# Optimization experiments

Measured on AMD Instinct MI355X. Metric: run time of the kernel, lower is better.

Reference implementation:

```python
import jax, jax.numpy as jnp
import numpy as np

B, S_SRC, S_TGT = 32, 64, 1024
D, H, DFF, LE, LD, V = 128, 8, 512, 6, 6, 64


def _pe(S, d):
    # PyTorch-style sinusoidal positional encoding, shape [S, d]
    pos = np.arange(S, dtype=np.float32)[:, None]
    div = np.exp(np.arange(0, d, 2, dtype=np.float32) * (-np.log(10000.0) / d))
    pe = np.zeros((S, d), dtype=np.float32)
    pe[:, 0::2] = np.sin(pos * div)
    pe[:, 1::2] = np.cos(pos * div)
    return jnp.asarray(pe)


def _ln(x, g, b, eps=1e-5):
    m = x.mean(-1, keepdims=True)
    v = ((x - m) ** 2).mean(-1, keepdims=True)
    return (x - m) / jnp.sqrt(v + eps) * g + b


def _mha(q_in, k_in, v_in, Wqkv, bqkv, Wo, bo):
    d = q_in.shape[-1]
    dh = d // H
    def proj(x, W, b):
        return (x @ W.T + b).reshape(x.shape[0], x.shape[1], H, dh)
    q = proj(q_in, Wqkv[:d], bqkv[:d])
    k = proj(k_in, Wqkv[d:2 * d], bqkv[d:2 * d])
    v = proj(v_in, Wqkv[2 * d:], bqkv[2 * d:])
    scores = jnp.einsum('bqhd,bkhd->bhqk', q, k) * (1.0 / np.sqrt(dh))
    a = jax.nn.softmax(scores, axis=-1)
    o = jnp.einsum('bhqk,bkhd->bqhd', a, v).reshape(q_in.shape[0], q_in.shape[1], d)
    return o @ Wo.T + bo


def _ffn(x, W1, b1, W2, b2):
    return jax.nn.relu(x @ W1.T + b1) @ W2.T + b2


def reference(src, tgt, emb,
              enc_qkv_w, enc_qkv_b, enc_out_w, enc_out_b,
              enc_ln1_g, enc_ln1_b, enc_ff1_w, enc_ff1_b,
              enc_ff2_w, enc_ff2_b, enc_ln2_g, enc_ln2_b,
              enc_norm_g, enc_norm_b,
              dec_sa_qkv_w, dec_sa_qkv_b, dec_sa_out_w, dec_sa_out_b,
              dec_ln1_g, dec_ln1_b,
              dec_ca_qkv_w, dec_ca_qkv_b, dec_ca_out_w, dec_ca_out_b,
              dec_ln2_g, dec_ln2_b,
              dec_ff1_w, dec_ff1_b, dec_ff2_w, dec_ff2_b,
              dec_ln3_g, dec_ln3_b, dec_norm_g, dec_norm_b,
              fc_w, fc_b):
    # src: [B, S_SRC] int tokens (occupation config); tgt: [B, S_TGT, D] (zeros in the original)
    s = emb[src] * np.sqrt(float(D)) + _pe(src.shape[1], D)
    t = tgt + _pe(tgt.shape[1], D)
    # encoder (post-norm, ReLU, dropout=0 in eval)
    for i in range(LE):
        s = _ln(s + _mha(s, s, s, enc_qkv_w[i], enc_qkv_b[i], enc_out_w[i], enc_out_b[i]),
                enc_ln1_g[i], enc_ln1_b[i])
        s = _ln(s + _ffn(s, enc_ff1_w[i], enc_ff1_b[i], enc_ff2_w[i], enc_ff2_b[i]),
                enc_ln2_g[i], enc_ln2_b[i])
    mem = _ln(s, enc_norm_g, enc_norm_b)
    # decoder
    for i in range(LD):
        t = _ln(t + _mha(t, t, t, dec_sa_qkv_w[i], dec_sa_qkv_b[i], dec_sa_out_w[i], dec_sa_out_b[i]),
                dec_ln1_g[i], dec_ln1_b[i])
        t = _ln(t + _mha(t, mem, mem, dec_ca_qkv_w[i], dec_ca_qkv_b[i], dec_ca_out_w[i], dec_ca_out_b[i]),
                dec_ln2_g[i], dec_ln2_b[i])
        t = _ln(t + _ffn(t, dec_ff1_w[i], dec_ff1_b[i], dec_ff2_w[i], dec_ff2_b[i]),
                dec_ln3_g[i], dec_ln3_b[i])
    t = _ln(t, dec_norm_g, dec_norm_b)
    return t @ fc_w.T + fc_b  # [B, S_TGT, 1] transformer correction to TN params


def setup_inputs():
    ks = iter(jax.random.split(jax.random.key(0), 64))
    def nrm(shape, scale=0.02):
        return jax.random.normal(next(ks), shape, dtype=jnp.float32) * scale
    inp = {
        'src': jax.random.randint(next(ks), (B, S_SRC), 0, V),
        'tgt': jnp.zeros((B, S_TGT, D), jnp.float32),
        'emb': nrm((V, D), 1.0),
        'enc_qkv_w': nrm((LE, 3 * D, D)), 'enc_qkv_b': jnp.zeros((LE, 3 * D)),
        'enc_out_w': nrm((LE, D, D)), 'enc_out_b': jnp.zeros((LE, D)),
        'enc_ln1_g': jnp.ones((LE, D)), 'enc_ln1_b': jnp.zeros((LE, D)),
        'enc_ff1_w': nrm((LE, DFF, D)), 'enc_ff1_b': jnp.zeros((LE, DFF)),
        'enc_ff2_w': nrm((LE, D, DFF)), 'enc_ff2_b': jnp.zeros((LE, D)),
        'enc_ln2_g': jnp.ones((LE, D)), 'enc_ln2_b': jnp.zeros((LE, D)),
        'enc_norm_g': jnp.ones((D,)), 'enc_norm_b': jnp.zeros((D,)),
        'dec_sa_qkv_w': nrm((LD, 3 * D, D)), 'dec_sa_qkv_b': jnp.zeros((LD, 3 * D)),
        'dec_sa_out_w': nrm((LD, D, D)), 'dec_sa_out_b': jnp.zeros((LD, D)),
        'dec_ln1_g': jnp.ones((LD, D)), 'dec_ln1_b': jnp.zeros((LD, D)),
        'dec_ca_qkv_w': nrm((LD, 3 * D, D)), 'dec_ca_qkv_b': jnp.zeros((LD, 3 * D)),
        'dec_ca_out_w': nrm((LD, D, D)), 'dec_ca_out_b': jnp.zeros((LD, D)),
        'dec_ln2_g': jnp.ones((LD, D)), 'dec_ln2_b': jnp.zeros((LD, D)),
        'dec_ff1_w': nrm((LD, DFF, D)), 'dec_ff1_b': jnp.zeros((LD, DFF)),
        'dec_ff2_w': nrm((LD, D, DFF)), 'dec_ff2_b': jnp.zeros((LD, D)),
        'dec_ln3_g': jnp.ones((LD, D)), 'dec_ln3_b': jnp.zeros((LD, D)),
        'dec_norm_g': jnp.ones((D,)), 'dec_norm_b': jnp.zeros((D,)),
        'fc_w': nrm((1, D)), 'fc_b': jnp.zeros((1,)),
    }
    return inp
```

## Files before the change

kernel.cpp:

```cpp
#include <hip/hip_runtime.h>
#include <hip/hip_bf16.h>
#include <stdint.h>

#define NH 8

typedef uint16_t u16;
typedef uint32_t u32;
typedef __attribute__((ext_vector_type(8))) short s8b;
typedef __attribute__((ext_vector_type(4))) float f32x4;
typedef __attribute__((ext_vector_type(16))) float f32x16;

#if __has_builtin(__builtin_amdgcn_exp2f)
#define EXPS(x) __builtin_amdgcn_exp2f(x)
#define QSCALE 0.36067376022224085f
#else
#define EXPS(x) __expf(x)
#define QSCALE 0.25f
#endif

__device__ __forceinline__ u16 f2b(float f) {
    u32 u = __builtin_bit_cast(u32, f);
    u = (u + 0x7fffu + ((u >> 16) & 1u)) >> 16;
    return (u16)u;
}

__device__ __forceinline__ u32 pkbf(float a, float b) {
    u32 ua = __builtin_bit_cast(u32, a) + 0x8000u;
    u32 ub = __builtin_bit_cast(u32, b) + 0x8000u;
    return __builtin_amdgcn_perm(ub, ua, 0x07060302);
}

__device__ __forceinline__ float pe_val(int pos, int d) {
    int j = d >> 1;
    float div = expf((float)j * -0.14391156831212787f);
    float ang = (float)pos * div;
    return (d & 1) ? cosf(ang) : sinf(ang);
}

__global__ void embed_kernel(const int* __restrict__ src, const float* __restrict__ emb,
                             float* __restrict__ S, u16* __restrict__ Sb) {
    int idx = blockIdx.x * 256 + threadIdx.x;
    int d = idx & 127;
    int n = idx >> 7;
    int i = n & 63;
    int tok = src[n];
    float v = emb[tok * 128 + d] * 11.313708498984761f + pe_val(i, d);
    S[idx] = v; Sb[idx] = f2b(v);
}

__global__ void addpe_kernel(const float* __restrict__ tgt, float* __restrict__ T,
                             u16* __restrict__ Tb) {
    int idx = blockIdx.x * 256 + threadIdx.x;
    int d = idx & 127;
    int n = idx >> 7;
    int i = n & 1023;
    float v = tgt[idx] + pe_val(i, d);
    T[idx] = v; Tb[idx] = f2b(v);
}

struct CvtJobs { const float* src[10]; u16* dst[10]; int n[10]; };
__global__ void cvt_kernel(CvtJobs jb) {
    int e = blockIdx.y;
    int i = blockIdx.x * 256 + threadIdx.x;
    if (i < jb.n[e]) jb.dst[e][i] = f2b(jb.src[e][i]);
}

__global__ void transposeV(const u16* __restrict__ KV, int stride, int voff,
                           u16* __restrict__ VT, int SKV) {
    int bh = blockIdx.x;
    int k0 = blockIdx.y * 64;
    int l = threadIdx.x;
    int b = bh >> 3, h = bh & 7;
    const u16* p = KV + (size_t)(b * SKV + k0 + l) * stride + voff + h * 16;
    s8b v0 = *(const s8b*)p;
    s8b v1 = *(const s8b*)(p + 8);
    size_t obase = (size_t)bh * 16 * SKV + k0 + l;
#pragma unroll
    for (int n = 0; n < 8; n++) VT[obase + (size_t)n * SKV] = (u16)v0[n];
#pragma unroll
    for (int n = 0; n < 8; n++) VT[obase + (size_t)(n + 8) * SKV] = (u16)v1[n];
}

template <int RELU>
__global__ __launch_bounds__(256) void gemm_mfma(const u16* __restrict__ A,
                                                 const u16* __restrict__ W,
                                                 const float* __restrict__ bias,
                                                 u16* __restrict__ C,
                                                 int M, int N, int K,
                                                 float qscale, int qcols) {
    __shared__ __align__(16) u16 As[128 * 56];
    __shared__ __align__(16) u16 Bs[128 * 56];
    int tid = threadIdx.x;
    int lane = tid & 63, w = tid >> 6;
    int quad = lane >> 4, l15 = lane & 15;
    int m0 = blockIdx.y * 128, n0 = blockIdx.x * 128;
    int wm = (w & 1) * 64, wn = (w >> 1) * 64;
    int srow = tid >> 1, skof = (tid & 1) * 16;

    f32x4 acc[4][4];
#pragma unroll
    for (int i = 0; i < 4; i++)
#pragma unroll
        for (int j = 0; j < 4; j++)
#pragma unroll
            for (int r = 0; r < 4; r++) acc[i][j][r] = 0.f;

    for (int k0 = 0; k0 < K; k0 += 32) {
        const u16* ga = A + (size_t)(m0 + srow) * K + k0 + skof;
        const u16* gw = W + (size_t)(n0 + srow) * K + k0 + skof;
        s8b a0 = *(const s8b*)ga, a1 = *(const s8b*)(ga + 8);
        s8b w0 = *(const s8b*)gw, w1 = *(const s8b*)(gw + 8);
        __syncthreads();
        *(s8b*)(As + srow * 56 + skof) = a0;
        *(s8b*)(As + srow * 56 + skof + 8) = a1;
        *(s8b*)(Bs + srow * 56 + skof) = w0;
        *(s8b*)(Bs + srow * 56 + skof + 8) = w1;
        __syncthreads();
        s8b af[4], bfr[4];
#pragma unroll
        for (int i = 0; i < 4; i++) af[i] = *(const s8b*)(As + (wm + 16 * i + l15) * 56 + quad * 8);
#pragma unroll
        for (int j = 0; j < 4; j++) bfr[j] = *(const s8b*)(Bs + (wn + 16 * j + l15) * 56 + quad * 8);
#pragma unroll
        for (int i = 0; i < 4; i++)
#pragma unroll
            for (int j = 0; j < 4; j++)
                acc[i][j] = __builtin_amdgcn_mfma_f32_16x16x32_bf16(af[i], bfr[j], acc[i][j], 0, 0, 0);
    }
#pragma unroll
    for (int j = 0; j < 4; j++) {
        int col = n0 + wn + 16 * j + l15;
        float bv = bias[col];
        float sc = (col < qcols) ? qscale : 1.f;
#pragma unroll
        for (int i = 0; i < 4; i++) {
            int rbase = m0 + wm + 16 * i + quad * 4;
#pragma unroll
            for (int r = 0; r < 4; r++) {
                float v = (acc[i][j][r] + bv) * sc;
                if (RELU) v = fmaxf(v, 0.f);
                C[(size_t)(rbase + r) * N + col] = f2b(v);
            }
        }
    }
}

__global__ __launch_bounds__(256) void gemm_ln(const u16* __restrict__ A,
                                               const u16* __restrict__ W,
                                               const float* __restrict__ bias,
                                               const float* __restrict__ X,
                                               const float* __restrict__ g,
                                               const float* __restrict__ bta,
                                               float* __restrict__ Y,
                                               u16* __restrict__ Yb,
                                               int M, int K) {
    __shared__ __align__(16) u16 As[128 * 56];
    __shared__ __align__(16) u16 Bs[128 * 56];
    __shared__ float redS[128][2], redQ[128][2];
    int tid = threadIdx.x;
    int lane = tid & 63, w = tid >> 6;
    int quad = lane >> 4, l15 = lane & 15;
    int m0 = blockIdx.x * 128;
    int wm = (w & 1) * 64, wn = (w >> 1) * 64;
    int srow = tid >> 1, skof = (tid & 1) * 16;

    f32x4 acc[4][4];
#pragma unroll
    for (int i = 0; i < 4; i++)
#pragma unroll
        for (int j = 0; j < 4; j++)
#pragma unroll
            for (int r = 0; r < 4; r++) acc[i][j][r] = 0.f;

    for (int k0 = 0; k0 < K; k0 += 32) {
        const u16* ga = A + (size_t)(m0 + srow) * K + k0 + skof;
        const u16* gw = W + (size_t)srow * K + k0 + skof;
        s8b a0 = *(const s8b*)ga, a1 = *(const s8b*)(ga + 8);
        s8b w0 = *(const s8b*)gw, w1 = *(const s8b*)(gw + 8);
        __syncthreads();
        *(s8b*)(As + srow * 56 + skof) = a0;
        *(s8b*)(As + srow * 56 + skof + 8) = a1;
        *(s8b*)(Bs + srow * 56 + skof) = w0;
        *(s8b*)(Bs + srow * 56 + skof + 8) = w1;
        __syncthreads();
        s8b af[4], bfr[4];
#pragma unroll
        for (int i = 0; i < 4; i++) af[i] = *(const s8b*)(As + (wm + 16 * i + l15) * 56 + quad * 8);
#pragma unroll
        for (int j = 0; j < 4; j++) bfr[j] = *(const s8b*)(Bs + (wn + 16 * j + l15) * 56 + quad * 8);
#pragma unroll
        for (int i = 0; i < 4; i++)
#pragma unroll
            for (int j = 0; j < 4; j++)
                acc[i][j] = __builtin_amdgcn_mfma_f32_16x16x32_bf16(af[i], bfr[j], acc[i][j], 0, 0, 0);
    }

    float s_[4][4], q_[4][4];
#pragma unroll
    for (int i = 0; i < 4; i++)
#pragma unroll
        for (int r = 0; r < 4; r++) {
            int row = m0 + wm + 16 * i + quad * 4 + r;
            float s = 0.f, q = 0.f;
#pragma unroll
            for (int j = 0; j < 4; j++) {
                int col = wn + 16 * j + l15;
                float x = acc[i][j][r] + bias[col] + X[(size_t)row * 128 + col];
                acc[i][j][r] = x;
                s += x; q += x * x;
            }
#pragma unroll
            for (int off = 1; off < 16; off <<= 1) {
                s += __shfl_xor(s, off);
                q += __shfl_xor(q, off);
            }
            s_[i][r] = s; q_[i][r] = q;
        }
    if (l15 == 0) {
#pragma unroll
        for (int i = 0; i < 4; i++)
#pragma unroll
            for (int r = 0; r < 4; r++) {
                int lrow = wm + 16 * i + quad * 4 + r;
                redS[lrow][wn >> 6] = s_[i][r];
                redQ[lrow][wn >> 6] = q_[i][r];
            }
    }
    __syncthreads();
#pragma unroll
    for (int i = 0; i < 4; i++)
#pragma unroll
        for (int r = 0; r < 4; r++) {
            int lrow = wm + 16 * i + quad * 4 + r;
            int row = m0 + lrow;
            float S2 = redS[lrow][0] + redS[lrow][1];
            float Q2 = redQ[lrow][0] + redQ[lrow][1];
            float mean = S2 * (1.f / 128.f);
            float var = Q2 * (1.f / 128.f) - mean * mean;
            float rstd = rsqrtf(var + 1e-5f);
#pragma unroll
            for (int j = 0; j < 4; j++) {
                int col = wn + 16 * j + l15;
                float y = (acc[i][j][r] - mean) * rstd * g[col] + bta[col];
                Y[(size_t)row * 128 + col] = y;
                Yb[(size_t)row * 128 + col] = f2b(y);
            }
        }
}

template <int WAVES>
__global__ __launch_bounds__(WAVES * 64) void attn3(
    const u16* __restrict__ Qb, int qstride, int qoff,
    const u16* __restrict__ Kb, int kstride, int koff,
    const u16* __restrict__ VT,
    u16* __restrict__ O, int SQ, int SKV) {
    __shared__ __align__(16) u32 Ps[WAVES][32 * 20];
    int tid = threadIdx.x;
    int lane = tid & 63, w = tid >> 6;
    int quad = lane >> 4, l15 = lane & 15, l31 = lane & 31, half = lane >> 5;
    int nqc = SQ / (WAVES * 32);
    int bid = blockIdx.x;
    int qc = bid % nqc;
    int h = (bid / nqc) % NH;
    int b = bid / (nqc * NH);
    int q0 = qc * WAVES * 32 + w * 32;

    const u16* qp = Qb + (size_t)(b * SQ + q0 + l31) * qstride + qoff + h * 16 + half * 8;
    s8b qf = *(const s8b*)qp;
    s8b ones;
#pragma unroll
    for (int j = 0; j < 8; j++) ones[j] = (short)0x3F80;

    const u16* vtb = VT + ((size_t)(b * NH + h) * 16 + l15) * SKV + quad * 8;
    const u16* kp = Kb + (size_t)(b * SKV + l31) * kstride + koff + h * 16 + half * 8;
    size_t kadv = (size_t)32 * kstride;

    f32x4 O0, O1, L0, L1;
#pragma unroll
    for (int r = 0; r < 4; r++) { O0[r] = 0.f; O1[r] = 0.f; L0[r] = 0.f; L1[r] = 0.f; }

    u32* pw = Ps[w];
#pragma unroll 2
    for (int j0 = 0; j0 < SKV; j0 += 32) {
        s8b kf = *(const s8b*)kp;
        kp += kadv;
        s8b vb = *(const s8b*)(vtb + j0);
        f32x16 S;
#pragma unroll
        for (int r = 0; r < 16; r++) S[r] = 0.f;
        S = __builtin_amdgcn_mfma_f32_32x32x16_bf16(kf, qf, S, 0, 0, 0);
#pragma unroll
        for (int g = 0; g < 4; g++) {
            float p0 = EXPS(S[4 * g + 0]);
            float p1 = EXPS(S[4 * g + 1]);
            float p2 = EXPS(S[4 * g + 2]);
            float p3 = EXPS(S[4 * g + 3]);
            int kw = l31 * 20 + 2 * half + 4 * g;
            pw[kw] = pkbf(p0, p1);
            pw[kw + 1] = pkbf(p2, p3);
        }
        __builtin_amdgcn_wave_barrier();
        s8b pa0 = *(const s8b*)(pw + l15 * 20 + quad * 4);
        s8b pa1 = *(const s8b*)(pw + (16 + l15) * 20 + quad * 4);
        O0 = __builtin_amdgcn_mfma_f32_16x16x32_bf16(pa0, vb, O0, 0, 0, 0);
        O1 = __builtin_amdgcn_mfma_f32_16x16x32_bf16(pa1, vb, O1, 0, 0, 0);
        L0 = __builtin_amdgcn_mfma_f32_16x16x32_bf16(pa0, ones, L0, 0, 0, 0);
        L1 = __builtin_amdgcn_mfma_f32_16x16x32_bf16(pa1, ones, L1, 0, 0, 0);
    }
#pragma unroll
    for (int r = 0; r < 4; r++) {
        int q = b * SQ + q0 + quad * 4 + r;
        O[(size_t)q * 128 + h * 16 + l15] = f2b(O0[r] / L0[r]);
        O[(size_t)(q + 16) * 128 + h * 16 + l15] = f2b(O1[r] / L1[r]);
    }
}

__global__ void ln_kernel(const float* __restrict__ X, const float* __restrict__ R,
                          const float* __restrict__ g, const float* __restrict__ bta,
                          float* __restrict__ Y, u16* __restrict__ Yb) {
    int r = blockIdx.x;
    int lane = threadIdx.x;
    size_t base = (size_t)r * 128;
    float x0 = X[base + lane], x1 = X[base + lane + 64];
    if (R) { x0 += R[base + lane]; x1 += R[base + lane + 64]; }
    float s = x0 + x1;
    for (int off = 32; off; off >>= 1) s += __shfl_xor(s, off);
    float mean = s * (1.f / 128.f);
    float d0 = x0 - mean, d1 = x1 - mean;
    float vs = d0 * d0 + d1 * d1;
    for (int off = 32; off; off >>= 1) vs += __shfl_xor(vs, off);
    float rstd = rsqrtf(vs * (1.f / 128.f) + 1e-5f);
    float y0 = d0 * rstd * g[lane] + bta[lane];
    float y1 = d1 * rstd * g[lane + 64] + bta[lane + 64];
    Y[base + lane] = y0;
    Y[base + lane + 64] = y1;
    if (Yb) { Yb[base + lane] = f2b(y0); Yb[base + lane + 64] = f2b(y1); }
}

__global__ void fc_kernel(const float* __restrict__ X, const float* __restrict__ w,
                          const float* __restrict__ b, float* __restrict__ out) {
    int r = blockIdx.x;
    int lane = threadIdx.x;
    size_t base = (size_t)r * 128;
    float s = X[base + lane] * w[lane] + X[base + lane + 64] * w[lane + 64];
    for (int off = 32; off; off >>= 1) s += __shfl_xor(s, off);
    if (lane == 0) out[r] = s + b[0];
}

static inline void gemm_b(const u16* A, const u16* W, const float* bias, u16* C,
                          int M, int N, int K, hipStream_t st, int qcols = 0) {
    hipLaunchKernelGGL((gemm_mfma<0>), dim3(N / 128, M / 128), dim3(256), 0, st,
                       A, W, bias, C, M, N, K, QSCALE, qcols);
}
static inline void gemm_br(const u16* A, const u16* W, const float* bias, u16* C,
                           int M, int N, int K, hipStream_t st) {
    hipLaunchKernelGGL((gemm_mfma<1>), dim3(N / 128, M / 128), dim3(256), 0, st,
                       A, W, bias, C, M, N, K, 1.f, 0);
}
static inline void gemmln(const u16* A, const u16* W, const float* bias,
                          const float* X, const float* g, const float* bta,
                          float* Y, u16* Yb, int M, int K, hipStream_t st) {
    hipLaunchKernelGGL(gemm_ln, dim3(M / 128), dim3(256), 0, st,
                       A, W, bias, X, g, bta, Y, Yb, M, K);
}

extern "C" void kernel_launch(void* const* d_in, const int* in_sizes, int n_in,
                              void* d_out, int out_size, void* d_ws, size_t ws_size,
                              hipStream_t stream) {
    const int B = 32, SSRC = 64, STGT = 1024, D = 128, DFF_ = 512, LE = 6, LD = 6;

    const int*   src = (const int*)d_in[0];
    const float* tgt = (const float*)d_in[1];
    const float* emb = (const float*)d_in[2];
    const float* enc_qkv_w = (const float*)d_in[3];
    const float* enc_qkv_b = (const float*)d_in[4];
    const float* enc_out_w = (const float*)d_in[5];
    const float* enc_out_b = (const float*)d_in[6];
    const float* enc_ln1_g = (const float*)d_in[7];
    const float* enc_ln1_b = (const float*)d_in[8];
    const float* enc_ff1_w = (const float*)d_in[9];
    const float* enc_ff1_b = (const float*)d_in[10];
    const float* enc_ff2_w = (const float*)d_in[11];
    const float* enc_ff2_b = (const float*)d_in[12];
    const float* enc_ln2_g = (const float*)d_in[13];
    const float* enc_ln2_b = (const float*)d_in[14];
    const float* enc_norm_g = (const float*)d_in[15];
    const float* enc_norm_b = (const float*)d_in[16];
    const float* dec_sa_qkv_w = (const float*)d_in[17];
    const float* dec_sa_qkv_b = (const float*)d_in[18];
    const float* dec_sa_out_w = (const float*)d_in[19];
    const float* dec_sa_out_b = (const float*)d_in[20];
    const float* dec_ln1_g = (const float*)d_in[21];
    const float* dec_ln1_b = (const float*)d_in[22];
    const float* dec_ca_qkv_w = (const float*)d_in[23];
    const float* dec_ca_qkv_b = (const float*)d_in[24];
    const float* dec_ca_out_w = (const float*)d_in[25];
    const float* dec_ca_out_b = (const float*)d_in[26];
    const float* dec_ln2_g = (const float*)d_in[27];
    const float* dec_ln2_b = (const float*)d_in[28];
    const float* dec_ff1_w = (const float*)d_in[29];
    const float* dec_ff1_b = (const float*)d_in[30];
    const float* dec_ff2_w = (const float*)d_in[31];
    const float* dec_ff2_b = (const float*)d_in[32];
    const float* dec_ln3_g = (const float*)d_in[33];
    const float* dec_ln3_b = (const float*)d_in[34];
    const float* dec_norm_g = (const float*)d_in[35];
    const float* dec_norm_b = (const float*)d_in[36];
    const float* fc_w = (const float*)d_in[37];
    const float* fc_b = (const float*)d_in[38];

    const int NT = B * STGT;
    const int NS = B * SSRC;

    float* t_f   = (float*)d_ws;
    float* s_f   = t_f + (size_t)NT * D;
    float* mem_f = s_f + (size_t)NS * D;
    u16* t_bf    = (u16*)(mem_f + (size_t)NS * D);
    u16* s_bf    = t_bf + (size_t)NT * D;
    u16* mem_bf  = s_bf + (size_t)NS * D;
    u16* qkv_bf  = mem_bf + (size_t)NS * D;
    u16* attno_bf = qkv_bf + (size_t)NT * DFF_;
    u16* ckv_bf  = attno_bf + (size_t)NT * D;
    u16* vt      = ckv_bf + (size_t)NS * 2 * D;
    u16* wa      = vt + (size_t)B * NH * 16 * STGT;

    u16* w_enc_qkv = wa;                          int n_enc_qkv = LE * 3 * D * D;
    u16* w_enc_out = w_enc_qkv + n_enc_qkv;       int n_enc_out = LE * D * D;
    u16* w_enc_ff1 = w_enc_out + n_enc_out;       int n_enc_ff1 = LE * DFF_ * D;
    u16* w_enc_ff2 = w_enc_ff1 + n_enc_ff1;       int n_enc_ff2 = LE * D * DFF_;
    u16* w_sa_qkv  = w_enc_ff2 + n_enc_ff2;       int n_sa_qkv = LD * 3 * D * D;
    u16* w_sa_out  = w_sa_qkv + n_sa_qkv;         int n_sa_out = LD * D * D;
    u16* w_ca_qkv  = w_sa_out + n_sa_out;         int n_ca_qkv = LD * 3 * D * D;
    u16* w_ca_out  = w_ca_qkv + n_ca_qkv;         int n_ca_out = LD * D * D;
    u16* w_ff1     = w_ca_out + n_ca_out;         int n_ff1 = LD * DFF_ * D;
    u16* w_ff2     = w_ff1 + n_ff1;               int n_ff2 = LD * D * DFF_;

    float* scf = (float*)qkv_bf;

    CvtJobs jb;
    jb.src[0] = enc_qkv_w;    jb.dst[0] = w_enc_qkv; jb.n[0] = n_enc_qkv;
    jb.src[1] = enc_out_w;    jb.dst[1] = w_enc_out; jb.n[1] = n_enc_out;
    jb.src[2] = enc_ff1_w;    jb.dst[2] = w_enc_ff1; jb.n[2] = n_enc_ff1;
    jb.src[3] = enc_ff2_w;    jb.dst[3] = w_enc_ff2; jb.n[3] = n_enc_ff2;
    jb.src[4] = dec_sa_qkv_w; jb.dst[4] = w_sa_qkv;  jb.n[4] = n_sa_qkv;
    jb.src[5] = dec_sa_out_w; jb.dst[5] = w_sa_out;  jb.n[5] = n_sa_out;
    jb.src[6] = dec_ca_qkv_w; jb.dst[6] = w_ca_qkv;  jb.n[6] = n_ca_qkv;
    jb.src[7] = dec_ca_out_w; jb.dst[7] = w_ca_out;  jb.n[7] = n_ca_out;
    jb.src[8] = dec_ff1_w;    jb.dst[8] = w_ff1;     jb.n[8] = n_ff1;
    jb.src[9] = dec_ff2_w;    jb.dst[9] = w_ff2;     jb.n[9] = n_ff2;
    int maxn = n_enc_ff1;
    hipLaunchKernelGGL(cvt_kernel, dim3((maxn + 255) / 256, 10), dim3(256), 0, stream, jb);

    hipLaunchKernelGGL(embed_kernel, dim3(NS * D / 256), dim3(256), 0, stream, src, emb, s_f, s_bf);

    for (int i = 0; i < LE; i++) {
        gemm_b(s_bf, w_enc_qkv + (size_t)i * 3 * D * D, enc_qkv_b + (size_t)i * 3 * D,
               qkv_bf, NS, 3 * D, D, stream, 128);
        hipLaunchKernelGGL(transposeV, dim3(B * NH, 1), dim3(64), 0, stream,
                           qkv_bf, 3 * D, 2 * D, vt, SSRC);
        hipLaunchKernelGGL((attn3<2>), dim3(B * NH), dim3(128), 0, stream,
                           qkv_bf, 3 * D, 0, qkv_bf, 3 * D, D, vt, attno_bf, SSRC, SSRC);
        gemmln(attno_bf, w_enc_out + (size_t)i * D * D, enc_out_b + (size_t)i * D,
               s_f, enc_ln1_g + (size_t)i * D, enc_ln1_b + (size_t)i * D, s_f, s_bf, NS, D, stream);
        gemm_br(s_bf, w_enc_ff1 + (size_t)i * DFF_ * D, enc_ff1_b + (size_t)i * DFF_,
                qkv_bf, NS, DFF_, D, stream);
        gemmln(qkv_bf, w_enc_ff2 + (size_t)i * D * DFF_, enc_ff2_b + (size_t)i * D,
               s_f, enc_ln2_g + (size_t)i * D, enc_ln2_b + (size_t)i * D, s_f, s_bf, NS, DFF_, stream);
    }
    hipLaunchKernelGGL(ln_kernel, dim3(NS), dim3(64), 0, stream,
                       s_f, (const float*)nullptr, enc_norm_g, enc_norm_b, mem_f, mem_bf);

    hipLaunchKernelGGL(addpe_kernel, dim3(NT * D / 256), dim3(256), 0, stream, tgt, t_f, t_bf);

    for (int i = 0; i < LD; i++) {
        gemm_b(t_bf, w_sa_qkv + (size_t)i * 3 * D * D, dec_sa_qkv_b + (size_t)i * 3 * D,
               qkv_bf, NT, 3 * D, D, stream, 128);
        hipLaunchKernelGGL(transposeV, dim3(B * NH, STGT / 64), dim3(64), 0, stream,
                           qkv_bf, 3 * D, 2 * D, vt, STGT);
        hipLaunchKernelGGL((attn3<4>), dim3(B * NH * (STGT / 128)), dim3(256), 0, stream,
                           qkv_bf, 3 * D, 0, qkv_bf, 3 * D, D, vt, attno_bf, STGT, STGT);
        gemmln(attno_bf, w_sa_out + (size_t)i * D * D, dec_sa_out_b + (size_t)i * D,
               t_f, dec_ln1_g + (size_t)i * D, dec_ln1_b + (size_t)i * D, t_f, t_bf, NT, D, stream);

        gemm_b(t_bf, w_ca_qkv + (size_t)i * 3 * D * D, dec_ca_qkv_b + (size_t)i * 3 * D,
               qkv_bf, NT, D, D, stream, 128);
        gemm_b(mem_bf, w_ca_qkv + (size_t)i * 3 * D * D + (size_t)D * D,
               dec_ca_qkv_b + (size_t)i * 3 * D + D, ckv_bf, NS, 2 * D, D, stream);
        hipLaunchKernelGGL(transposeV, dim3(B * NH, 1), dim3(64), 0, stream,
                           ckv_bf, 2 * D, D, vt, SSRC);
        hipLaunchKernelGGL((attn3<4>), dim3(B * NH * (STGT / 128)), dim3(256), 0, stream,
                           qkv_bf, D, 0, ckv_bf, 2 * D, 0, vt, attno_bf, STGT, SSRC);
        gemmln(attno_bf, w_ca_out + (size_t)i * D * D, dec_ca_out_b + (size_t)i * D,
               t_f, dec_ln2_g + (size_t)i * D, dec_ln2_b + (size_t)i * D, t_f, t_bf, NT, D, stream);

        gemm_br(t_bf, w_ff1 + (size_t)i * DFF_ * D, dec_ff1_b + (size_t)i * DFF_,
                qkv_bf, NT, DFF_, D, stream);
        gemmln(qkv_bf, w_ff2 + (size_t)i * D * DFF_, dec_ff2_b + (size_t)i * D,
               t_f, dec_ln3_g + (size_t)i * D, dec_ln3_b + (size_t)i * D, t_f, t_bf, NT, DFF_, stream);
    }

    hipLaunchKernelGGL(ln_kernel, dim3(NT), dim3(64), 0, stream,
                       t_f, (const float*)nullptr, dec_norm_g, dec_norm_b, scf, (u16*)nullptr);
    hipLaunchKernelGGL(fc_kernel, dim3(NT), dim3(64), 0, stream,
                       scf, fc_w, fc_b, (float*)d_out);
}
```

Measured before the change: 1.508 ms.

## Drop LDS staging in GEMMs, fuse V transpose into QKV epilogue, smaller encoder tiles

The GEMM kernels now load MFMA fragments straight from global memory into registers instead of staging tiles through shared memory with two barriers per K step. The QKV projection epilogue writes the V block directly in transposed per-head layout, which removes the separate transposeV launches. A templated tile shape gives the small encoder GEMMs (M=2048) 32-row tiles so more blocks are launched. Direct global loads give up shared-memory reuse and rely on L1/L2 hits, and the transposed V stores are scattered 4-byte writes.

```diff
diff --git a/kernel.cpp b/kernel.cpp
--- a/kernel.cpp
+++ b/kernel.cpp
@@ -65,76 +65,70 @@
     if (i < jb.n[e]) jb.dst[e][i] = f2b(jb.src[e][i]);
 }
 
-__global__ void transposeV(const u16* __restrict__ KV, int stride, int voff,
-                           u16* __restrict__ VT, int SKV) {
-    int bh = blockIdx.x;
-    int k0 = blockIdx.y * 64;
-    int l = threadIdx.x;
-    int b = bh >> 3, h = bh & 7;
-    const u16* p = KV + (size_t)(b * SKV + k0 + l) * stride + voff + h * 16;
-    s8b v0 = *(const s8b*)p;
-    s8b v1 = *(const s8b*)(p + 8);
-    size_t obase = (size_t)bh * 16 * SKV + k0 + l;
-#pragma unroll
-    for (int n = 0; n < 8; n++) VT[obase + (size_t)n * SKV] = (u16)v0[n];
-#pragma unroll
-    for (int n = 0; n < 8; n++) VT[obase + (size_t)(n + 8) * SKV] = (u16)v1[n];
-}
-
-template <int RELU>
-__global__ __launch_bounds__(256) void gemm_mfma(const u16* __restrict__ A,
-                                                 const u16* __restrict__ W,
-                                                 const float* __restrict__ bias,
-                                                 u16* __restrict__ C,
-                                                 int M, int N, int K,
-                                                 float qscale, int qcols) {
-    __shared__ __align__(16) u16 As[128 * 56];
-    __shared__ __align__(16) u16 Bs[128 * 56];
+template <int AI, int BJ, int WM, int WN, int RELU>
+__global__ __launch_bounds__(64 * WM * WN) void gemm_direct(
+    const u16* __restrict__ A, const u16* __restrict__ W,
+    const float* __restrict__ bias, u16* __restrict__ C,
+    int M, int N, int K, float qscale, int qcols,
+    u16* __restrict__ vt, int vcol0, int sshift, int smask, int skv) {
     int tid = threadIdx.x;
     int lane = tid & 63, w = tid >> 6;
     int quad = lane >> 4, l15 = lane & 15;
-    int m0 = blockIdx.y * 128, n0 = blockIdx.x * 128;
-    int wm = (w & 1) * 64, wn = (w >> 1) * 64;
-    int srow = tid >> 1, skof = (tid & 1) * 16;
-
-    f32x4 acc[4][4];
-#pragma unroll
-    for (int i = 0; i < 4; i++)
-#pragma unroll
-        for (int j = 0; j < 4; j++)
+    int wmi = w % WM, wni = w / WM;
+    int m0 = blockIdx.y * (16 * AI * WM), n0 = blockIdx.x * (16 * BJ * WN);
+    int mb = m0 + wmi * 16 * AI, nb = n0 + wni * 16 * BJ;
+
+    const u16* Ab = A + (size_t)(mb + l15) * K + quad * 8;
+    const u16* Wb = W + (size_t)(nb + l15) * K + quad * 8;
+
+    f32x4 acc[AI][BJ];
+#pragma unroll
+    for (int i = 0; i < AI; i++)
+#pragma unroll
+        for (int j = 0; j < BJ; j++)
 #pragma unroll
             for (int r = 0; r < 4; r++) acc[i][j][r] = 0.f;
 
+#pragma unroll 2
     for (int k0 = 0; k0 < K; k0 += 32) {
-        const u16* ga = A + (size_t)(m0 + srow) * K + k0 + skof;
-        const u16* gw = W + (size_t)(n0 + srow) * K + k0 + skof;
-        s8b a0 = *(const s8b*)ga, a1 = *(const s8b*)(ga + 8);
-        s8b w0 = *(const s8b*)gw, w1 = *(const s8b*)(gw + 8);
-        __syncthreads();
-        *(s8b*)(As + srow * 56 + skof) = a0;
-        *(s8b*)(As + srow * 56 + skof + 8) = a1;
-        *(s8b*)(Bs + srow * 56 + skof) = w0;
-        *(s8b*)(Bs + srow * 56 + skof + 8) = w1;
-        __syncthreads();
-        s8b af[4], bfr[4];
-#pragma unroll
-        for (int i = 0; i < 4; i++) af[i] = *(const s8b*)(As + (wm + 16 * i + l15) * 56 + quad * 8);
-#pragma unroll
-        for (int j = 0; j < 4; j++) bfr[j] = *(const s8b*)(Bs + (wn + 16 * j + l15) * 56 + quad * 8);
-#pragma unroll
-        for (int i = 0; i < 4; i++)
-#pragma unroll
-            for (int j = 0; j < 4; j++)
-                acc[i][j] = __builtin_amdgcn_mfma_f32_16x16x32_bf16(af[i], bfr[j], acc[i][j], 0, 0, 0);
-    }
-#pragma unroll
-    for (int j = 0; j < 4; j++) {
-        int col = n0 + wn + 16 * j + l15;
+        s8b af[AI], bf[BJ];
+#pragma unroll
+        for (int i = 0; i < AI; i++) af[i] = *(const s8b*)(Ab + (size_t)16 * i * K + k0);
+#pragma unroll
+        for (int j = 0; j < BJ; j++) bf[j] = *(const s8b*)(Wb + (size_t)16 * j * K + k0);
+#pragma unroll
+        for (int i = 0; i < AI; i++)
+#pragma unroll
+            for (int j = 0; j < BJ; j++)
+                acc[i][j] = __builtin_amdgcn_mfma_f32_16x16x32_bf16(af[i], bf[j], acc[i][j], 0, 0, 0);
+    }
+
+    if (vt && n0 == vcol0) {
+#pragma unroll
+        for (int j = 0; j < BJ; j++) {
+            int lc = wni * 16 * BJ + 16 * j + l15;
+            int h = lc >> 4, n = lc & 15;
+            float bv = bias[vcol0 + lc];
+#pragma unroll
+            for (int i = 0; i < AI; i++) {
+                int row = mb + 16 * i + quad * 4;
+                int b = row >> sshift, tok = row & smask;
+                u32 lo = pkbf(acc[i][j][0] + bv, acc[i][j][1] + bv);
+                u32 hi = pkbf(acc[i][j][2] + bv, acc[i][j][3] + bv);
+                u32* p = (u32*)(vt + ((size_t)((b * 8 + h) * 16 + n)) * skv + tok);
+                p[0] = lo; p[1] = hi;
+            }
+        }
+        return;
+    }
+#pragma unroll
+    for (int j = 0; j < BJ; j++) {
+        int col = nb + 16 * j + l15;
         float bv = bias[col];
         float sc = (col < qcols) ? qscale : 1.f;
 #pragma unroll
-        for (int i = 0; i < 4; i++) {
-            int rbase = m0 + wm + 16 * i + quad * 4;
+        for (int i = 0; i < AI; i++) {
+            int rbase = mb + 16 * i + quad * 4;
 #pragma unroll
             for (int r = 0; r < 4; r++) {
                 float v = (acc[i][j][r] + bv) * sc;
@@ -145,66 +139,54 @@
     }
 }
 
-__global__ __launch_bounds__(256) void gemm_ln(const u16* __restrict__ A,
-                                               const u16* __restrict__ W,
-                                               const float* __restrict__ bias,
-                                               const float* __restrict__ X,
-                                               const float* __restrict__ g,
-                                               const float* __restrict__ bta,
-                                               float* __restrict__ Y,
-                                               u16* __restrict__ Yb,
-                                               int M, int K) {
-    __shared__ __align__(16) u16 As[128 * 56];
-    __shared__ __align__(16) u16 Bs[128 * 56];
-    __shared__ float redS[128][2], redQ[128][2];
+template <int AI, int BJ, int WM, int WN>
+__global__ __launch_bounds__(64 * WM * WN) void gemm_ln_t(
+    const u16* __restrict__ A, const u16* __restrict__ W,
+    const float* __restrict__ bias, const float* __restrict__ X,
+    const float* __restrict__ g, const float* __restrict__ bta,
+    float* __restrict__ Y, u16* __restrict__ Yb, int M, int K) {
+    __shared__ float redS[16 * AI * WM][WN], redQ[16 * AI * WM][WN];
     int tid = threadIdx.x;
     int lane = tid & 63, w = tid >> 6;
     int quad = lane >> 4, l15 = lane & 15;
-    int m0 = blockIdx.x * 128;
-    int wm = (w & 1) * 64, wn = (w >> 1) * 64;
-    int srow = tid >> 1, skof = (tid & 1) * 16;
-
-    f32x4 acc[4][4];
-#pragma unroll
-    for (int i = 0; i < 4; i++)
-#pragma unroll
-        for (int j = 0; j < 4; j++)
+    int wmi = w % WM, wni = w / WM;
+    int m0 = blockIdx.x * (16 * AI * WM);
+    int mb = m0 + wmi * 16 * AI, nb = wni * 16 * BJ;
+
+    const u16* Ab = A + (size_t)(mb + l15) * K + quad * 8;
+    const u16* Wb = W + (size_t)(nb + l15) * K + quad * 8;
+
+    f32x4 acc[AI][BJ];
+#pragma unroll
+    for (int i = 0; i < AI; i++)
+#pragma unroll
+        for (int j = 0; j < BJ; j++)
 #pragma unroll
             for (int r = 0; r < 4; r++) acc[i][j][r] = 0.f;
 
+#pragma unroll 2
     for (int k0 = 0; k0 < K; k0 += 32) {
-        const u16* ga = A + (size_t)(m0 + srow) * K + k0 + skof;
-        const u16* gw = W + (size_t)srow * K + k0 + skof;
-        s8b a0 = *(const s8b*)ga, a1 = *(const s8b*)(ga + 8);
-        s8b w0 = *(const s8b*)gw, w1 = *(const s8b*)(gw + 8);
-        __syncthreads();
-        *(s8b*)(As + srow * 56 + skof) = a0;
-        *(s8b*)(As + srow * 56 + skof + 8) = a1;
-        *(s8b*)(Bs + srow * 56 + skof) = w0;
-        *(s8b*)(Bs + srow * 56 + skof + 8) = w1;
-        __syncthreads();
-        s8b af[4], bfr[4];
-#pragma unroll
-        for (int i = 0; i < 4; i++) af[i] = *(const s8b*)(As + (wm + 16 * i + l15) * 56 + quad * 8);
-#pragma unroll
-        for (int j = 0; j < 4; j++) bfr[j] = *(const s8b*)(Bs + (wn + 16 * j + l15) * 56 + quad * 8);
-#pragma unroll
-        for (int i = 0; i < 4; i++)
-#pragma unroll
-            for (int j = 0; j < 4; j++)
-                acc[i][j] = __builtin_amdgcn_mfma_f32_16x16x32_bf16(af[i], bfr[j], acc[i][j], 0, 0, 0);
-    }
-
-    float s_[4][4], q_[4][4];
-#pragma unroll
-    for (int i = 0; i < 4; i++)
+        s8b af[AI], bf[BJ];
+#pragma unroll
+        for (int i = 0; i < AI; i++) af[i] = *(const s8b*)(Ab + (size_t)16 * i * K + k0);
+#pragma unroll
+        for (int j = 0; j < BJ; j++) bf[j] = *(const s8b*)(Wb + (size_t)16 * j * K + k0);
+#pragma unroll
+        for (int i = 0; i < AI; i++)
+#pragma unroll
+            for (int j = 0; j < BJ; j++)
+                acc[i][j] = __builtin_amdgcn_mfma_f32_16x16x32_bf16(af[i], bf[j], acc[i][j], 0, 0, 0);
+    }
+
+#pragma unroll
+    for (int i = 0; i < AI; i++)
 #pragma unroll
         for (int r = 0; r < 4; r++) {
-            int row = m0 + wm + 16 * i + quad * 4 + r;
+            int row = mb + 16 * i + quad * 4 + r;
             float s = 0.f, q = 0.f;
 #pragma unroll
-            for (int j = 0; j < 4; j++) {
-                int col = wn + 16 * j + l15;
+            for (int j = 0; j < BJ; j++) {
+                int col = nb + 16 * j + l15;
                 float x = acc[i][j][r] + bias[col] + X[(size_t)row * 128 + col];
                 acc[i][j][r] = x;
                 s += x; q += x * x;
@@ -214,33 +196,28 @@
                 s += __shfl_xor(s, off);
                 q += __shfl_xor(q, off);
             }
-            s_[i][r] = s; q_[i][r] = q;
+            if (l15 == 0) {
+                int lrow = wmi * 16 * AI + 16 * i + quad * 4 + r;
+                redS[lrow][wni] = s;
+                redQ[lrow][wni] = q;
+            }
         }
-    if (l15 == 0) {
-#pragma unroll
-        for (int i = 0; i < 4; i++)
-#pragma unroll
-            for (int r = 0; r < 4; r++) {
-                int lrow = wm + 16 * i + quad * 4 + r;
-                redS[lrow][wn >> 6] = s_[i][r];
-                redQ[lrow][wn >> 6] = q_[i][r];
-            }
-    }
     __syncthreads();
 #pragma unroll
-    for (int i = 0; i < 4; i++)
+    for (int i = 0; i < AI; i++)
 #pragma unroll
         for (int r = 0; r < 4; r++) {
-            int lrow = wm + 16 * i + quad * 4 + r;
+            int lrow = wmi * 16 * AI + 16 * i + quad * 4 + r;
             int row = m0 + lrow;
-            float S2 = redS[lrow][0] + redS[lrow][1];
-            float Q2 = redQ[lrow][0] + redQ[lrow][1];
+            float S2 = 0.f, Q2 = 0.f;
+#pragma unroll
+            for (int u = 0; u < WN; u++) { S2 += redS[lrow][u]; Q2 += redQ[lrow][u]; }
             float mean = S2 * (1.f / 128.f);
             float var = Q2 * (1.f / 128.f) - mean * mean;
             float rstd = rsqrtf(var + 1e-5f);
 #pragma unroll
-            for (int j = 0; j < 4; j++) {
-                int col = wn + 16 * j + l15;
+            for (int j = 0; j < BJ; j++) {
+                int col = nb + 16 * j + l15;
                 float y = (acc[i][j][r] - mean) * rstd * g[col] + bta[col];
                 Y[(size_t)row * 128 + col] = y;
                 Yb[(size_t)row * 128 + col] = f2b(y);
@@ -347,20 +324,38 @@
     if (lane == 0) out[r] = s + b[0];
 }
 
-static inline void gemm_b(const u16* A, const u16* W, const float* bias, u16* C,
-                          int M, int N, int K, hipStream_t st, int qcols = 0) {
-    hipLaunchKernelGGL((gemm_mfma<0>), dim3(N / 128, M / 128), dim3(256), 0, st,
-                       A, W, bias, C, M, N, K, QSCALE, qcols);
-}
-static inline void gemm_br(const u16* A, const u16* W, const float* bias, u16* C,
-                           int M, int N, int K, hipStream_t st) {
-    hipLaunchKernelGGL((gemm_mfma<1>), dim3(N / 128, M / 128), dim3(256), 0, st,
-                       A, W, bias, C, M, N, K, 1.f, 0);
-}
-static inline void gemmln(const u16* A, const u16* W, const float* bias,
-                          const float* X, const float* g, const float* bta,
-                          float* Y, u16* Yb, int M, int K, hipStream_t st) {
-    hipLaunchKernelGGL(gemm_ln, dim3(M / 128), dim3(256), 0, st,
+static inline void gemmD(const u16* A, const u16* W, const float* bias, u16* C,
+                         int M, int N, int K, hipStream_t st, int qcols = 0,
+                         u16* vt = nullptr, int vcol0 = 0, int sshift = 0, int skv = 0) {
+    hipLaunchKernelGGL((gemm_direct<4, 4, 2, 2, 0>), dim3(N / 128, M / 128), dim3(256), 0, st,
+                       A, W, bias, C, M, N, K, QSCALE, qcols, vt, vcol0, sshift, (1 << sshift) - 1, skv);
+}
+static inline void gemmDr(const u16* A, const u16* W, const float* bias, u16* C,
+                          int M, int N, int K, hipStream_t st) {
+    hipLaunchKernelGGL((gemm_direct<4, 4, 2, 2, 1>), dim3(N / 128, M / 128), dim3(256), 0, st,
+                       A, W, bias, C, M, N, K, 1.f, 0, (u16*)nullptr, 0, 0, 0, 0);
+}
+static inline void gemmE(const u16* A, const u16* W, const float* bias, u16* C,
+                         int M, int N, int K, hipStream_t st, int qcols = 0,
+                         u16* vt = nullptr, int vcol0 = 0, int sshift = 0, int skv = 0) {
+    hipLaunchKernelGGL((gemm_direct<2, 2, 1, 4, 0>), dim3(N / 128, M / 32), dim3(256), 0, st,
+                       A, W, bias, C, M, N, K, QSCALE, qcols, vt, vcol0, sshift, (1 << sshift) - 1, skv);
+}
+static inline void gemmEr(const u16* A, const u16* W, const float* bias, u16* C,
+                          int M, int N, int K, hipStream_t st) {
+    hipLaunchKernelGGL((gemm_direct<2, 2, 1, 4, 1>), dim3(N / 128, M / 32), dim3(256), 0, st,
+                       A, W, bias, C, M, N, K, 1.f, 0, (u16*)nullptr, 0, 0, 0, 0);
+}
+static inline void gemmlnD(const u16* A, const u16* W, const float* bias,
+                           const float* X, const float* g, const float* bta,
+                           float* Y, u16* Yb, int M, int K, hipStream_t st) {
+    hipLaunchKernelGGL((gemm_ln_t<4, 4, 2, 2>), dim3(M / 128), dim3(256), 0, st,
+                       A, W, bias, X, g, bta, Y, Yb, M, K);
+}
+static inline void gemmlnE(const u16* A, const u16* W, const float* bias,
+                           const float* X, const float* g, const float* bta,
+                           float* Y, u16* Yb, int M, int K, hipStream_t st) {
+    hipLaunchKernelGGL((gemm_ln_t<2, 2, 1, 4>), dim3(M / 32), dim3(256), 0, st,
                        A, W, bias, X, g, bta, Y, Yb, M, K);
 }
 
@@ -454,18 +449,16 @@
     hipLaunchKernelGGL(embed_kernel, dim3(NS * D / 256), dim3(256), 0, stream, src, emb, s_f, s_bf);
 
     for (int i = 0; i < LE; i++) {
-        gemm_b(s_bf, w_enc_qkv + (size_t)i * 3 * D * D, enc_qkv_b + (size_t)i * 3 * D,
-               qkv_bf, NS, 3 * D, D, stream, 128);
-        hipLaunchKernelGGL(transposeV, dim3(B * NH, 1), dim3(64), 0, stream,
-                           qkv_bf, 3 * D, 2 * D, vt, SSRC);
+        gemmE(s_bf, w_enc_qkv + (size_t)i * 3 * D * D, enc_qkv_b + (size_t)i * 3 * D,
+              qkv_bf, NS, 3 * D, D, stream, 128, vt, 256, 6, SSRC);
         hipLaunchKernelGGL((attn3<2>), dim3(B * NH), dim3(128), 0, stream,
                            qkv_bf, 3 * D, 0, qkv_bf, 3 * D, D, vt, attno_bf, SSRC, SSRC);
-        gemmln(attno_bf, w_enc_out + (size_t)i * D * D, enc_out_b + (size_t)i * D,
-               s_f, enc_ln1_g + (size_t)i * D, enc_ln1_b + (size_t)i * D, s_f, s_bf, NS, D, stream);
-        gemm_br(s_bf, w_enc_ff1 + (size_t)i * DFF_ * D, enc_ff1_b + (size_t)i * DFF_,
-                qkv_bf, NS, DFF_, D, stream);
-        gemmln(qkv_bf, w_enc_ff2 + (size_t)i * D * DFF_, enc_ff2_b + (size_t)i * D,
-               s_f, enc_ln2_g + (size_t)i * D, enc_ln2_b + (size_t)i * D, s_f, s_bf, NS, DFF_, stream);
+        gemmlnE(attno_bf, w_enc_out + (size_t)i * D * D, enc_out_b + (size_t)i * D,
+                s_f, enc_ln1_g + (size_t)i * D, enc_ln1_b + (size_t)i * D, s_f, s_bf, NS, D, stream);
+        gemmEr(s_bf, w_enc_ff1 + (size_t)i * DFF_ * D, enc_ff1_b + (size_t)i * DFF_,
+               qkv_bf, NS, DFF_, D, stream);
+        gemmlnE(qkv_bf, w_enc_ff2 + (size_t)i * D * DFF_, enc_ff2_b + (size_t)i * D,
+                s_f, enc_ln2_g + (size_t)i * D, enc_ln2_b + (size_t)i * D, s_f, s_bf, NS, DFF_, stream);
     }
     hipLaunchKernelGGL(ln_kernel, dim3(NS), dim3(64), 0, stream,
                        s_f, (const float*)nullptr, enc_norm_g, enc_norm_b, mem_f, mem_bf);
@@ -473,30 +466,27 @@
     hipLaunchKernelGGL(addpe_kernel, dim3(NT * D / 256), dim3(256), 0, stream, tgt, t_f, t_bf);
 
     for (int i = 0; i < LD; i++) {
-        gemm_b(t_bf, w_sa_qkv + (size_t)i * 3 * D * D, dec_sa_qkv_b + (size_t)i * 3 * D,
-               qkv_bf, NT, 3 * D, D, stream, 128);
-        hipLaunchKernelGGL(transposeV, dim3(B * NH, STGT / 64), dim3(64), 0, stream,
-                           qkv_bf, 3 * D, 2 * D, vt, STGT);
+        gemmD(t_bf, w_sa_qkv + (size_t)i * 3 * D * D, dec_sa_qkv_b + (size_t)i * 3 * D,
+              qkv_bf, NT, 3 * D, D, stream, 128, vt, 256, 10, STGT);
         hipLaunchKernelGGL((attn3<4>), dim3(B * NH * (STGT / 128)), dim3(256), 0, stream,
                            qkv_bf, 3 * D, 0, qkv_bf, 3 * D, D, vt, attno_bf, STGT, STGT);
-        gemmln(attno_bf, w_sa_out + (size_t)i * D * D, dec_sa_out_b + (size_t)i * D,
-               t_f, dec_ln1_g + (size_t)i * D, dec_ln1_b + (size_t)i * D, t_f, t_bf, NT, D, stream);
-
-        gemm_b(t_bf, w_ca_qkv + (size_t)i * 3 * D * D, dec_ca_qkv_b + (size_t)i * 3 * D,
-               qkv_bf, NT, D, D, stream, 128);
-        gemm_b(mem_bf, w_ca_qkv + (size_t)i * 3 * D * D + (size_t)D * D,
-               dec_ca_qkv_b + (size_t)i * 3 * D + D, ckv_bf, NS, 2 * D, D, stream);
-        hipLaunchKernelGGL(transposeV, dim3(B * NH, 1), dim3(64), 0, stream,
-                           ckv_bf, 2 * D, D, vt, SSRC);
+        gemmlnD(attno_bf, w_sa_out + (size_t)i * D * D, dec_sa_out_b + (size_t)i * D,
+                t_f, dec_ln1_g + (size_t)i * D, dec_ln1_b + (size_t)i * D, t_f, t_bf, NT, D, stream);
+
+        gemmD(t_bf, w_ca_qkv + (size_t)i * 3 * D * D, dec_ca_qkv_b + (size_t)i * 3 * D,
+              qkv_bf, NT, D, D, stream, 128);
+        gemmE(mem_bf, w_ca_qkv + (size_t)i * 3 * D * D + (size_t)D * D,
+              dec_ca_qkv_b + (size_t)i * 3 * D + D, ckv_bf, NS, 2 * D, D, stream,
+              0, vt, 128, 6, SSRC);
         hipLaunchKernelGGL((attn3<4>), dim3(B * NH * (STGT / 128)), dim3(256), 0, stream,
                            qkv_bf, D, 0, ckv_bf, 2 * D, 0, vt, attno_bf, STGT, SSRC);
-        gemmln(attno_bf, w_ca_out + (size_t)i * D * D, dec_ca_out_b + (size_t)i * D,
-               t_f, dec_ln2_g + (size_t)i * D, dec_ln2_b + (size_t)i * D, t_f, t_bf, NT, D, stream);
-
-        gemm_br(t_bf, w_ff1 + (size_t)i * DFF_ * D, dec_ff1_b + (size_t)i * DFF_,
-                qkv_bf, NT, DFF_, D, stream);
-        gemmln(qkv_bf, w_ff2 + (size_t)i * D * DFF_, dec_ff2_b + (size_t)i * D,
-               t_f, dec_ln3_g + (size_t)i * D, dec_ln3_b + (size_t)i * D, t_f, t_bf, NT, DFF_, stream);
+        gemmlnD(attno_bf, w_ca_out + (size_t)i * D * D, dec_ca_out_b + (size_t)i * D,
+                t_f, dec_ln2_g + (size_t)i * D, dec_ln2_b + (size_t)i * D, t_f, t_bf, NT, D, stream);
+
+        gemmDr(t_bf, w_ff1 + (size_t)i * DFF_ * D, dec_ff1_b + (size_t)i * DFF_,
+               qkv_bf, NT, DFF_, D, stream);
+        gemmlnD(qkv_bf, w_ff2 + (size_t)i * D * DFF_, dec_ff2_b + (size_t)i * D,
+                t_f, dec_ln3_g + (size_t)i * D, dec_ln3_b + (size_t)i * D, t_f, t_bf, NT, DFF_, stream);
     }
 
     hipLaunchKernelGGL(ln_kernel, dim3(NT), dim3(64), 0, stream,
```

Result: slower. 1.552 ms (+2.9%).
